# Optimization experiments

Measured on AMD Instinct MI355X. Metric: run time of the kernel, lower is better.

## Reference

```python
import jax, jax.numpy as jnp
import numpy as np
import math

B, N, DIM = 2, 4096, 1024
H, D, M = 16, 64, 256


def setup_inputs() -> dict:
    key = jax.random.key(0)
    ks = jax.random.split(key, 6)
    s = 1.0 / math.sqrt(DIM)
    return {
        "x": jax.random.normal(ks[0], (B, N, DIM), dtype=jnp.float32),
        "w_q": jax.random.normal(ks[1], (DIM, H * D), dtype=jnp.float32) * s,
        "w_k": jax.random.normal(ks[2], (DIM, H * D), dtype=jnp.float32) * s,
        "w_v": jax.random.normal(ks[3], (DIM, H * D), dtype=jnp.float32) * s,
        "w_o": jax.random.normal(ks[4], (H * D, DIM), dtype=jnp.float32) * s,
        "b_o": jnp.zeros((DIM,), dtype=jnp.float32),
        "omega": jax.random.normal(ks[5], (M, D), dtype=jnp.float32),
    }


def _heads(t):
    # [B, N, H*D] -> [B, H, N, D]
    return t.reshape(B, N, H, D).transpose(0, 2, 1, 3)


def _phi(t, omega):
    # t: [B,H,N,D], omega: [M,D] -> [B,H,N,M]
    proj = jnp.einsum("bhnd,md->bhnm", t, omega)
    norm = 0.5 * jnp.sum(t * t, axis=-1, keepdims=True)
    return jnp.exp(proj - norm) / math.sqrt(M)


def reference(x, w_q, w_k, w_v, w_o, b_o, omega):
    q = _heads(x @ w_q)
    k = _heads(x @ w_k)
    v = _heads(x @ w_v)
    phi_q = _phi(q, omega)          # [B,H,N,M]
    phi_k = _phi(k, omega)          # [B,H,N,M]
    kv = jnp.einsum("bhnm,bhnd->bhmd", phi_k, v)   # [B,H,M,D]
    k_sum = phi_k.sum(axis=2)                       # [B,H,M]
    z = 1.0 / (jnp.einsum("bhnm,bhm->bhn", phi_q, k_sum) + 1e-6)
    out = jnp.einsum("bhnm,bhmd->bhnd", phi_q, kv) * z[..., None]
    out = out.transpose(0, 2, 1, 3).reshape(B, N, H * D)
    return out @ w_o + b_o
```

## Files before the change

kernel.cpp:

```cpp
#include <hip/hip_runtime.h>

#define DEVI __device__ __forceinline__

using f32x4 = __attribute__((ext_vector_type(4))) float;
using fvec4 = __attribute__((ext_vector_type(4))) float;
using s16x4 = __attribute__((ext_vector_type(4))) short;
using s16x8 = __attribute__((ext_vector_type(8))) short;

DEVI unsigned short f2bf_rn(float f) {
  union { float f; unsigned u; } v; v.f = f;
  unsigned r = v.u + 0x7fffu + ((v.u >> 16) & 1u);
  return (unsigned short)(r >> 16);
}
DEVI float bf2f(unsigned short h) {
  union { unsigned u; float f; } v; v.u = ((unsigned)h) << 16;
  return v.f;
}
DEVI f32x4 mfma16(s16x8 a, s16x8 b, f32x4 c) {
  return __builtin_amdgcn_mfma_f32_16x16x32_bf16(a, b, c, 0, 0, 0);
}
DEVI void gld16(const void* g, void* lds) {
  __builtin_amdgcn_global_load_lds(
      (const __attribute__((address_space(1))) unsigned int*)g,
      (__attribute__((address_space(3))) unsigned int*)lds, 16, 0, 0);
}

__global__ __launch_bounds__(256) void k_split_x(
    const float* __restrict__ X,
    unsigned short* __restrict__ XH, unsigned short* __restrict__ XL)
{
  size_t i = ((size_t)blockIdx.x * 256 + threadIdx.x) * 8;
  fvec4 a = *(const fvec4*)&X[i];
  fvec4 b = *(const fvec4*)&X[i + 4];
  s16x8 hv, lv;
#pragma unroll
  for (int j = 0; j < 4; ++j) {
    unsigned short h = f2bf_rn(a[j]);
    hv[j] = (short)h; lv[j] = (short)f2bf_rn(a[j] - bf2f(h));
  }
#pragma unroll
  for (int j = 0; j < 4; ++j) {
    unsigned short h = f2bf_rn(b[j]);
    hv[4 + j] = (short)h; lv[4 + j] = (short)f2bf_rn(b[j] - bf2f(h));
  }
  *(s16x8*)&XH[i] = hv;
  *(s16x8*)&XL[i] = lv;
}

__global__ __launch_bounds__(256) void k_prep_w(
    const float* __restrict__ wq, const float* __restrict__ wk,
    const float* __restrict__ wv, const float* __restrict__ wo,
    const float* __restrict__ omega,
    unsigned short* __restrict__ WTh, unsigned short* __restrict__ WOT,
    unsigned short* __restrict__ OMB)
{
  __shared__ float tile[64][65];
  const int z = blockIdx.z;
  const int t = threadIdx.x;
  if (z == 4) {
    int bid = blockIdx.x * 16 + blockIdx.y;
    if (bid < 16) {
      int i = (bid * 256 + t) * 4;
      fvec4 v = *(const fvec4*)&omega[i];
      s16x4 hv;
#pragma unroll
      for (int q = 0; q < 4; ++q) hv[q] = (short)f2bf_rn(v[q]);
      *(s16x4*)&OMB[i] = hv;
    }
    return;
  }
  const float* src = (z == 0) ? wq : (z == 1) ? wk : (z == 2) ? wv : wo;
  const int k0 = blockIdx.x * 64;
  const int n0 = blockIdx.y * 64;
#pragma unroll
  for (int j = 0; j < 4; ++j) {
    int r = (t >> 4) + 16 * j;
    int c = (t & 15) * 4;
    fvec4 v = *(const fvec4*)&src[(size_t)(k0 + r) * 1024 + n0 + c];
#pragma unroll
    for (int i = 0; i < 4; ++i) tile[r][c + i] = v[i];
  }
  __syncthreads();
#pragma unroll
  for (int j = 0; j < 4; ++j) {
    int n = (t >> 4) + 16 * j;
    int kc = (t & 15) * 4;
    s16x4 hv;
#pragma unroll
    for (int i = 0; i < 4; ++i) hv[i] = (short)f2bf_rn(tile[kc + i][n]);
    if (z < 3) {
      *(s16x4*)&WTh[(size_t)(z * 1024 + n0 + n) * 1024 + k0 + kc] = hv;
    } else {
      *(s16x4*)&WOT[(size_t)(n0 + n) * 1024 + k0 + kc] = hv;
    }
  }
}

__global__ __launch_bounds__(256) void k_gemm_qkv(
    const unsigned short* __restrict__ XH, const unsigned short* __restrict__ XL,
    const unsigned short* __restrict__ WTh,
    unsigned short* __restrict__ QH, unsigned short* __restrict__ QL,
    unsigned short* __restrict__ KH, unsigned short* __restrict__ KL,
    unsigned short* __restrict__ VB)
{
  __shared__ unsigned short AH[3][128 * 32];
  __shared__ unsigned short BHs[3][128 * 32];
  __shared__ unsigned short AL[3][128 * 32];
  const int flat = blockIdx.y * 24 + blockIdx.x;
  const int swz = (flat & 7) * 192 + (flat >> 3);
  const int cb = swz % 24;
  const int rb = swz / 24;
  const int t = threadIdx.x;
  const int w = t >> 6, l = t & 63;
  const bool tp = (cb < 16);
  f32x4 acc[4][4];
#pragma unroll
  for (int a = 0; a < 4; ++a)
#pragma unroll
    for (int b = 0; b < 4; ++b) acc[a][b] = (f32x4)0.f;

  const int r0 = w * 32;
  const int lrow = l >> 2;
  const int lcol = (l & 3) * 8;
  const size_t gA = (size_t)(rb * 128 + r0 + lrow) * 1024 + lcol;
  const size_t gB = (size_t)(cb * 128 + r0 + lrow) * 1024 + lcol;
  const int lds0 = r0 * 32;
  const int lds1 = (r0 + 16) * 32;

  const int wm = (w & 1) * 64, wn = (w >> 1) * 64;
  const int lr = l & 15, ko = (l >> 4) * 8;

  auto STAGE = [&](int buf, int k0) {
    gld16(&XH[gA + k0], &AH[buf][lds0]);
    gld16(&XH[gA + (size_t)16 * 1024 + k0], &AH[buf][lds1]);
    if (tp) {
      gld16(&XL[gA + k0], &AL[buf][lds0]);
      gld16(&XL[gA + (size_t)16 * 1024 + k0], &AL[buf][lds1]);
    }
    gld16(&WTh[gB + k0], &BHs[buf][lds0]);
    gld16(&WTh[gB + (size_t)16 * 1024 + k0], &BHs[buf][lds1]);
  };

  STAGE(0, 0);
  STAGE(1, 32);
  int cur = 0;
  for (int ks = 0; ks < 32; ++ks) {
    if (ks < 30) {
      int nxt = (cur >= 1) ? cur - 1 : 2;
      STAGE(nxt, (ks + 2) * 32);
      if (tp) asm volatile("s_waitcnt vmcnt(12)" ::: "memory");
      else    asm volatile("s_waitcnt vmcnt(8)" ::: "memory");
    } else if (ks == 30) {
      if (tp) asm volatile("s_waitcnt vmcnt(6)" ::: "memory");
      else    asm volatile("s_waitcnt vmcnt(4)" ::: "memory");
    } else {
      asm volatile("s_waitcnt vmcnt(0)" ::: "memory");
    }
    __builtin_amdgcn_s_barrier();
    asm volatile("" ::: "memory");
    s16x8 ah[4], al[4], bh[4];
#pragma unroll
    for (int f = 0; f < 4; ++f) {
      ah[f] = *(const s16x8*)&AH[cur][(wm + f * 16 + lr) * 32 + ko];
      bh[f] = *(const s16x8*)&BHs[cur][(wn + f * 16 + lr) * 32 + ko];
    }
    if (tp) {
#pragma unroll
      for (int f = 0; f < 4; ++f) al[f] = *(const s16x8*)&AL[cur][(wm + f * 16 + lr) * 32 + ko];
    }
#pragma unroll
    for (int fa = 0; fa < 4; ++fa)
#pragma unroll
      for (int fb = 0; fb < 4; ++fb) {
        acc[fa][fb] = mfma16(ah[fa], bh[fb], acc[fa][fb]);
        if (tp) acc[fa][fb] = mfma16(al[fa], bh[fb], acc[fa][fb]);
      }
    asm volatile("s_waitcnt lgkmcnt(0)" ::: "memory");
    __builtin_amdgcn_s_barrier();
    asm volatile("" ::: "memory");
    cur = (cur < 2) ? cur + 1 : 0;
  }
  const int lg = l >> 4;
#pragma unroll
  for (int fa = 0; fa < 4; ++fa)
#pragma unroll
    for (int r = 0; r < 4; ++r) {
      int row = rb * 128 + wm + fa * 16 + lg * 4 + r;
#pragma unroll
      for (int fb = 0; fb < 4; ++fb) {
        int col = cb * 128 + wn + fb * 16 + lr;
        float v = acc[fa][fb][r];
        if (tp) {
          unsigned short hs = f2bf_rn(v);
          unsigned short ls = f2bf_rn(v - bf2f(hs));
          if (cb < 8) {
            QH[(size_t)row * 1024 + col] = hs;
            QL[(size_t)row * 1024 + col] = ls;
          } else {
            KH[(size_t)row * 1024 + col - 1024] = hs;
            KL[(size_t)row * 1024 + col - 1024] = ls;
          }
        } else {
          VB[(size_t)row * 1024 + col - 2048] = f2bf_rn(v);
        }
      }
    }
}

__global__ __launch_bounds__(512, 1) void k_phik_kv(
    const unsigned short* __restrict__ KH, const unsigned short* __restrict__ KL,
    const unsigned short* __restrict__ VB,
    const unsigned short* __restrict__ OMB, float* __restrict__ KVP)
{
  __shared__ unsigned short OH[256][72];
  __shared__ unsigned short KHs[64][72], KLs[64][72];
  __shared__ unsigned short PKT[256][72];
  __shared__ unsigned short AVT[80][72];
  __shared__ float norm_s[64];
  const int nc = blockIdx.x;
  const int bh = blockIdx.y;
  const int b = bh >> 4, h = bh & 15;
  const int t = threadIdx.x, w = t >> 6, l = t & 63;
  const int lr = l & 15, lg = l >> 4, ko8 = lg * 8;

#pragma unroll
  for (int j = 0; j < 4; ++j) {
    int idx = j * 512 + t;
    int m = idx >> 3, c = (idx & 7) * 8;
    *(s16x8*)&OH[m][c] = *(const s16x8*)&OMB[m * 64 + c];
  }
  for (int e = t; e < 16 * 64; e += 512) {
    int rr = e >> 6, cc = e & 63;
    AVT[64 + rr][cc] = (rr == 0) ? (unsigned short)0x3F80 : (unsigned short)0;
  }

  f32x4 acc2[5][2];
#pragma unroll
  for (int a = 0; a < 5; ++a)
#pragma unroll
    for (int bb = 0; bb < 2; ++bb) acc2[a][bb] = (f32x4)0.f;

  for (int st = 0; st < 8; ++st) {
    const int n0 = nc * 512 + st * 64;
    __syncthreads();
    {
      int r = t >> 3, c8 = (t & 7) * 8;
      size_t o = (size_t)(b * 4096 + n0 + r) * 1024 + h * 64 + c8;
      s16x8 vh = *(const s16x8*)&KH[o];
      s16x8 vl = *(const s16x8*)&KL[o];
      *(s16x8*)&KHs[r][c8] = vh;
      *(s16x8*)&KLs[r][c8] = vl;
      float ss = 0.f;
#pragma unroll
      for (int i = 0; i < 8; ++i) {
        float q = bf2f((unsigned short)vh[i]) + bf2f((unsigned short)vl[i]);
        ss += q * q;
      }
      ss += __shfl_xor(ss, 1);
      ss += __shfl_xor(ss, 2);
      ss += __shfl_xor(ss, 4);
      if ((t & 7) == 0) norm_s[r] = 0.5f * ss;
    }
    {
      int n = t >> 3, dq = (t & 7) * 8;
      s16x8 v = *(const s16x8*)&VB[(size_t)(b * 4096 + n0 + n) * 1024 + h * 64 + dq];
#pragma unroll
      for (int i = 0; i < 8; ++i) AVT[dq + i][n] = (unsigned short)v[i];
    }
    __syncthreads();
    f32x4 acc[4][2];
#pragma unroll
    for (int a = 0; a < 4; ++a)
#pragma unroll
      for (int bb = 0; bb < 2; ++bb) acc[a][bb] = (f32x4)0.f;
#pragma unroll
    for (int ksub = 0; ksub < 2; ++ksub) {
      int ko = ksub * 32 + ko8;
      s16x8 ah[4], al[4], bh[2];
#pragma unroll
      for (int f = 0; f < 4; ++f) {
        ah[f] = *(const s16x8*)&KHs[f * 16 + lr][ko];
        al[f] = *(const s16x8*)&KLs[f * 16 + lr][ko];
      }
#pragma unroll
      for (int f = 0; f < 2; ++f) bh[f] = *(const s16x8*)&OH[w * 32 + f * 16 + lr][ko];
#pragma unroll
      for (int fa = 0; fa < 4; ++fa)
#pragma unroll
        for (int fb = 0; fb < 2; ++fb) {
          acc[fa][fb] = mfma16(ah[fa], bh[fb], acc[fa][fb]);
          acc[fa][fb] = mfma16(al[fa], bh[fb], acc[fa][fb]);
        }
    }
#pragma unroll
    for (int fa = 0; fa < 4; ++fa)
#pragma unroll
      for (int r = 0; r < 4; ++r) {
        int n = fa * 16 + lg * 4 + r;
        float nm = norm_s[n];
#pragma unroll
        for (int fb = 0; fb < 2; ++fb) {
          int m = w * 32 + fb * 16 + lr;
          float p = __expf(acc[fa][fb][r] - nm) * 0.0625f;
          PKT[m][n] = f2bf_rn(p);
        }
      }
    __syncthreads();
#pragma unroll
    for (int ksub = 0; ksub < 2; ++ksub) {
      int ko = ksub * 32 + ko8;
      s16x8 fA[5], fB[2];
#pragma unroll
      for (int f = 0; f < 5; ++f) fA[f] = *(const s16x8*)&AVT[f * 16 + lr][ko];
#pragma unroll
      for (int f = 0; f < 2; ++f) fB[f] = *(const s16x8*)&PKT[w * 32 + f * 16 + lr][ko];
#pragma unroll
      for (int fa = 0; fa < 5; ++fa)
#pragma unroll
        for (int fb = 0; fb < 2; ++fb) acc2[fa][fb] = mfma16(fA[fa], fB[fb], acc2[fa][fb]);
    }
  }
#pragma unroll
  for (int fa = 0; fa < 5; ++fa)
#pragma unroll
    for (int r = 0; r < 4; ++r) {
      int dp = fa * 16 + lg * 4 + r;
#pragma unroll
      for (int fb = 0; fb < 2; ++fb) {
        int m = w * 32 + fb * 16 + lr;
        KVP[(size_t)((bh * 8 + nc) * 80 + dp) * 256 + m] = acc2[fa][fb][r];
      }
    }
}

__global__ __launch_bounds__(256) void k_kv_reduce(
    const float* __restrict__ KVP, unsigned short* __restrict__ KVTB)
{
  int idx = blockIdx.x * 256 + threadIdx.x;
  if (idx >= 32 * 80 * 256) return;
  int bh = idx / (80 * 256);
  int rem = idx % (80 * 256);
  float s = 0.f;
#pragma unroll
  for (int nci = 0; nci < 8; ++nci) s += KVP[(size_t)(bh * 8 + nci) * 80 * 256 + rem];
  KVTB[idx] = f2bf_rn(s);
}

__global__ __launch_bounds__(256) void k_phiq_attn(
    const unsigned short* QH, const unsigned short* QL,
    const unsigned short* __restrict__ OMB,
    const unsigned short* __restrict__ KVTB,
    unsigned short* ATT)
{
  __shared__ unsigned short QHs[64][72], QLs[64][72];
  __shared__ unsigned short OH[256][72];
  __shared__ unsigned short PQ[64][264];
  __shared__ unsigned short KVB[80][264];
  __shared__ float norm_s[64];
  const int nt = blockIdx.x;
  const int bh = blockIdx.y;
  const int t = threadIdx.x, w = t >> 6, l = t & 63;
  const int b = bh >> 4, h = bh & 15;
  const int lr = l & 15, lg = l >> 4, ko8 = lg * 8;

  {
    int r = t >> 2, cq = (t & 3) * 4;
    float ss = 0.f;
#pragma unroll
    for (int j = 0; j < 4; ++j) {
      int c = cq + 16 * j;
      size_t o = (size_t)(b * 4096 + nt * 64 + r) * 1024 + h * 64 + c;
      s16x4 vh = *(const s16x4*)&QH[o];
      s16x4 vl = *(const s16x4*)&QL[o];
      *(s16x4*)&QHs[r][c] = vh;
      *(s16x4*)&QLs[r][c] = vl;
#pragma unroll
      for (int i = 0; i < 4; ++i) {
        float q = bf2f((unsigned short)vh[i]) + bf2f((unsigned short)vl[i]);
        ss += q * q;
      }
    }
    ss += __shfl_xor(ss, 1);
    ss += __shfl_xor(ss, 2);
    if ((t & 3) == 0) norm_s[r] = 0.5f * ss;
  }
#pragma unroll
  for (int j = 0; j < 8; ++j) {
    int idx = j * 256 + t;
    int m = idx >> 3, c = (idx & 7) * 8;
    *(s16x8*)&OH[m][c] = *(const s16x8*)&OMB[m * 64 + c];
  }
#pragma unroll
  for (int j = 0; j < 10; ++j) {
    int e = (j * 256 + t) * 8;
    int dp = e >> 8, m = e & 255;
    *(s16x8*)&KVB[dp][m] = *(const s16x8*)&KVTB[(size_t)bh * 80 * 256 + dp * 256 + m];
  }
  __syncthreads();
  f32x4 acc[4][4];
#pragma unroll
  for (int a = 0; a < 4; ++a)
#pragma unroll
    for (int bb = 0; bb < 4; ++bb) acc[a][bb] = (f32x4)0.f;
#pragma unroll
  for (int ksub = 0; ksub < 2; ++ksub) {
    int ko = ksub * 32 + ko8;
    s16x8 ah[4], al[4], bh[4];
#pragma unroll
    for (int f = 0; f < 4; ++f) {
      ah[f] = *(const s16x8*)&QHs[f * 16 + lr][ko];
      al[f] = *(const s16x8*)&QLs[f * 16 + lr][ko];
      bh[f] = *(const s16x8*)&OH[w * 64 + f * 16 + lr][ko];
    }
#pragma unroll
    for (int fa = 0; fa < 4; ++fa)
#pragma unroll
      for (int fb = 0; fb < 4; ++fb) {
        acc[fa][fb] = mfma16(ah[fa], bh[fb], acc[fa][fb]);
        acc[fa][fb] = mfma16(al[fa], bh[fb], acc[fa][fb]);
      }
  }
#pragma unroll
  for (int fa = 0; fa < 4; ++fa)
#pragma unroll
    for (int r = 0; r < 4; ++r) {
      int n = fa * 16 + lg * 4 + r;
      float nm = norm_s[n];
#pragma unroll
      for (int fb = 0; fb < 4; ++fb) {
        int m = w * 64 + fb * 16 + lr;
        float p = __expf(acc[fa][fb][r] - nm) * 0.0625f;
        PQ[n][m] = f2bf_rn(p);
      }
    }
  __syncthreads();
  f32x4 acc2[5];
#pragma unroll
  for (int bb = 0; bb < 5; ++bb) acc2[bb] = (f32x4)0.f;
  for (int ks = 0; ks < 8; ++ks) {
    const int m0 = ks * 32;
    s16x8 fA = *(const s16x8*)&PQ[w * 16 + lr][m0 + ko8];
    s16x8 fB[5];
#pragma unroll
    for (int f = 0; f < 5; ++f) fB[f] = *(const s16x8*)&KVB[f * 16 + lr][m0 + ko8];
#pragma unroll
    for (int fb = 0; fb < 5; ++fb) acc2[fb] = mfma16(fA, fB[fb], acc2[fb]);
  }
#pragma unroll
  for (int r = 0; r < 4; ++r) {
    float den = __shfl(acc2[4][r], (l & 48));
    float z = 1.f / (den + 1e-6f);
    int n = nt * 64 + w * 16 + lg * 4 + r;
#pragma unroll
    for (int fb = 0; fb < 4; ++fb) {
      int col = h * 64 + fb * 16 + lr;
      ATT[(size_t)(b * 4096 + n) * 1024 + col] = f2bf_rn(acc2[fb][r] * z);
    }
  }
}

__global__ __launch_bounds__(256) void k_gemm_out(
    const unsigned short* __restrict__ ATT,
    const unsigned short* __restrict__ WOT,
    const float* __restrict__ b_o,
    float* __restrict__ OUT)
{
  __shared__ unsigned short As[3][128 * 32], Bs[3][128 * 32];
  const int flat = blockIdx.y * 8 + blockIdx.x;
  const int swz = (flat & 7) * 64 + (flat >> 3);
  const int cb = swz % 8;
  const int rb = swz / 8;
  const int t = threadIdx.x, w = t >> 6, l = t & 63;
  f32x4 acc[4][4];
#pragma unroll
  for (int a = 0; a < 4; ++a)
#pragma unroll
    for (int bb = 0; bb < 4; ++bb) acc[a][bb] = (f32x4)0.f;

  const int r0 = w * 32;
  const int lrow = l >> 2;
  const int lcol = (l & 3) * 8;
  const size_t gA = (size_t)(rb * 128 + r0 + lrow) * 1024 + lcol;
  const size_t gB = (size_t)(cb * 128 + r0 + lrow) * 1024 + lcol;
  const int lds0 = r0 * 32;
  const int lds1 = (r0 + 16) * 32;

  const int wm = (w & 1) * 64, wn = (w >> 1) * 64;
  const int lr = l & 15, ko = (l >> 4) * 8;

  auto STAGE = [&](int buf, int k0) {
    gld16(&ATT[gA + k0], &As[buf][lds0]);
    gld16(&ATT[gA + (size_t)16 * 1024 + k0], &As[buf][lds1]);
    gld16(&WOT[gB + k0], &Bs[buf][lds0]);
    gld16(&WOT[gB + (size_t)16 * 1024 + k0], &Bs[buf][lds1]);
  };

  STAGE(0, 0);
  STAGE(1, 32);
  int cur = 0;
  for (int ks = 0; ks < 32; ++ks) {
    if (ks < 30) {
      int nxt = (cur >= 1) ? cur - 1 : 2;
      STAGE(nxt, (ks + 2) * 32);
      asm volatile("s_waitcnt vmcnt(8)" ::: "memory");
    } else if (ks == 30) {
      asm volatile("s_waitcnt vmcnt(4)" ::: "memory");
    } else {
      asm volatile("s_waitcnt vmcnt(0)" ::: "memory");
    }
    __builtin_amdgcn_s_barrier();
    asm volatile("" ::: "memory");
    s16x8 fA[4], fB[4];
#pragma unroll
    for (int f = 0; f < 4; ++f) {
      fA[f] = *(const s16x8*)&As[cur][(wm + f * 16 + lr) * 32 + ko];
      fB[f] = *(const s16x8*)&Bs[cur][(wn + f * 16 + lr) * 32 + ko];
    }
#pragma unroll
    for (int fa = 0; fa < 4; ++fa)
#pragma unroll
      for (int fb = 0; fb < 4; ++fb) acc[fa][fb] = mfma16(fA[fa], fB[fb], acc[fa][fb]);
    asm volatile("s_waitcnt lgkmcnt(0)" ::: "memory");
    __builtin_amdgcn_s_barrier();
    asm volatile("" ::: "memory");
    cur = (cur < 2) ? cur + 1 : 0;
  }
  const int lg = l >> 4;
#pragma unroll
  for (int fa = 0; fa < 4; ++fa)
#pragma unroll
    for (int r = 0; r < 4; ++r) {
      int row = rb * 128 + wm + fa * 16 + lg * 4 + r;
#pragma unroll
      for (int fb = 0; fb < 4; ++fb) {
        int col = cb * 128 + wn + fb * 16 + lr;
        OUT[(size_t)row * 1024 + col] = acc[fa][fb][r] + b_o[col];
      }
    }
}

extern "C" void kernel_launch(void* const* d_in, const int* in_sizes, int n_in,
                              void* d_out, int out_size, void* d_ws, size_t ws_size,
                              hipStream_t stream)
{
  const float* x  = (const float*)d_in[0];
  const float* wq = (const float*)d_in[1];
  const float* wk = (const float*)d_in[2];
  const float* wv = (const float*)d_in[3];
  const float* wo = (const float*)d_in[4];
  const float* bo = (const float*)d_in[5];
  const float* om = (const float*)d_in[6];
  float* out = (float*)d_out;

  const size_t PLANE = (size_t)8192 * 1024 * 2;
  char* ws = (char*)d_ws;
  unsigned short* WOT = (unsigned short*)(ws);
  char* segB = ws + 2097152;
  char* segC = segB + 2 * PLANE;
  char* segD = segC + 4 * PLANE;
  char* segE = segD + 26214400;

  unsigned short* QH  = (unsigned short*)segB;
  unsigned short* QL  = (unsigned short*)(segB + PLANE);
  unsigned short* ATT = (unsigned short*)segB;

  unsigned short* KH  = (unsigned short*)segC;
  unsigned short* KL  = (unsigned short*)(segC + PLANE);
  unsigned short* VB  = (unsigned short*)(segC + 2 * PLANE);
  unsigned short* XH  = (unsigned short*)(segC + 3 * PLANE);

  unsigned short* WTh = (unsigned short*)segD;
  unsigned short* XL  = (unsigned short*)(segD + 6291456);
  float* KVP = (float*)segD;
  unsigned short* KVTB = (unsigned short*)segE;
  unsigned short* OMB  = (unsigned short*)(segE + 1310720);

  k_split_x<<<dim3(4096), 256, 0, stream>>>(x, XH, XL);
  k_prep_w<<<dim3(16, 16, 5), 256, 0, stream>>>(wq, wk, wv, wo, om, WTh, WOT, OMB);
  k_gemm_qkv<<<dim3(24, 64), 256, 0, stream>>>(XH, XL, WTh, QH, QL, KH, KL, VB);
  k_phik_kv<<<dim3(8, 32), 512, 0, stream>>>(KH, KL, VB, OMB, KVP);
  k_kv_reduce<<<dim3(2560), 256, 0, stream>>>(KVP, KVTB);
  k_phiq_attn<<<dim3(64, 32), 256, 0, stream>>>(QH, QL, OMB, KVTB, ATT);
  k_gemm_out<<<dim3(8, 64), 256, 0, stream>>>(ATT, WOT, bo, out);
}
```

Baseline: 242.3 us.

## Shrink QKV GEMM to double buffering and load omega/KV fragments directly to registers

The QKV GEMM drops from a three-stage to a two-stage LDS ring, which lowers LDS use but shortens how far global loads run ahead of compute. In the phi_k and phi_q kernels, omega MFMA fragments now load straight from global memory into registers, so the OH shared tiles are gone. In the phi_q attention kernel, KV fragments are read from global/L2 inside the k-loop instead of being staged in LDS. This cuts LDS footprint and staging cost, which may raise occupancy, at the price of more global loads with less latency hiding.

```diff
diff --git a/kernel.cpp b/kernel.cpp
--- a/kernel.cpp
+++ b/kernel.cpp
@@ -103,9 +103,9 @@
     unsigned short* __restrict__ KH, unsigned short* __restrict__ KL,
     unsigned short* __restrict__ VB)
 {
-  __shared__ unsigned short AH[3][128 * 32];
-  __shared__ unsigned short BHs[3][128 * 32];
-  __shared__ unsigned short AL[3][128 * 32];
+  __shared__ unsigned short AH[2][128 * 32];
+  __shared__ unsigned short BHs[2][128 * 32];
+  __shared__ unsigned short AL[2][128 * 32];
   const int flat = blockIdx.y * 24 + blockIdx.x;
   const int swz = (flat & 7) * 192 + (flat >> 3);
   const int cb = swz % 24;
@@ -142,15 +142,10 @@
   };
 
   STAGE(0, 0);
-  STAGE(1, 32);
   int cur = 0;
   for (int ks = 0; ks < 32; ++ks) {
-    if (ks < 30) {
-      int nxt = (cur >= 1) ? cur - 1 : 2;
-      STAGE(nxt, (ks + 2) * 32);
-      if (tp) asm volatile("s_waitcnt vmcnt(12)" ::: "memory");
-      else    asm volatile("s_waitcnt vmcnt(8)" ::: "memory");
-    } else if (ks == 30) {
+    if (ks < 31) {
+      STAGE(cur ^ 1, (ks + 1) * 32);
       if (tp) asm volatile("s_waitcnt vmcnt(6)" ::: "memory");
       else    asm volatile("s_waitcnt vmcnt(4)" ::: "memory");
     } else {
@@ -178,7 +173,7 @@
     asm volatile("s_waitcnt lgkmcnt(0)" ::: "memory");
     __builtin_amdgcn_s_barrier();
     asm volatile("" ::: "memory");
-    cur = (cur < 2) ? cur + 1 : 0;
+    cur ^= 1;
   }
   const int lg = l >> 4;
 #pragma unroll
@@ -212,7 +207,6 @@
     const unsigned short* __restrict__ VB,
     const unsigned short* __restrict__ OMB, float* __restrict__ KVP)
 {
-  __shared__ unsigned short OH[256][72];
   __shared__ unsigned short KHs[64][72], KLs[64][72];
   __shared__ unsigned short PKT[256][72];
   __shared__ unsigned short AVT[80][72];
@@ -223,12 +217,13 @@
   const int t = threadIdx.x, w = t >> 6, l = t & 63;
   const int lr = l & 15, lg = l >> 4, ko8 = lg * 8;
 
-#pragma unroll
-  for (int j = 0; j < 4; ++j) {
-    int idx = j * 512 + t;
-    int m = idx >> 3, c = (idx & 7) * 8;
-    *(s16x8*)&OH[m][c] = *(const s16x8*)&OMB[m * 64 + c];
-  }
+  s16x8 omf[2][2];
+#pragma unroll
+  for (int ksub = 0; ksub < 2; ++ksub)
+#pragma unroll
+    for (int f = 0; f < 2; ++f)
+      omf[ksub][f] = *(const s16x8*)&OMB[(w * 32 + f * 16 + lr) * 64 + ksub * 32 + ko8];
+
   for (int e = t; e < 16 * 64; e += 512) {
     int rr = e >> 6, cc = e & 63;
     AVT[64 + rr][cc] = (rr == 0) ? (unsigned short)0x3F80 : (unsigned short)0;
@@ -276,20 +271,18 @@
 #pragma unroll
     for (int ksub = 0; ksub < 2; ++ksub) {
       int ko = ksub * 32 + ko8;
-      s16x8 ah[4], al[4], bh[2];
+      s16x8 ah[4], al[4];
 #pragma unroll
       for (int f = 0; f < 4; ++f) {
         ah[f] = *(const s16x8*)&KHs[f * 16 + lr][ko];
         al[f] = *(const s16x8*)&KLs[f * 16 + lr][ko];
       }
 #pragma unroll
-      for (int f = 0; f < 2; ++f) bh[f] = *(const s16x8*)&OH[w * 32 + f * 16 + lr][ko];
-#pragma unroll
       for (int fa = 0; fa < 4; ++fa)
 #pragma unroll
         for (int fb = 0; fb < 2; ++fb) {
-          acc[fa][fb] = mfma16(ah[fa], bh[fb], acc[fa][fb]);
-          acc[fa][fb] = mfma16(al[fa], bh[fb], acc[fa][fb]);
+          acc[fa][fb] = mfma16(ah[fa], omf[ksub][fb], acc[fa][fb]);
+          acc[fa][fb] = mfma16(al[fa], omf[ksub][fb], acc[fa][fb]);
         }
     }
 #pragma unroll
@@ -353,15 +346,20 @@
     unsigned short* ATT)
 {
   __shared__ unsigned short QHs[64][72], QLs[64][72];
-  __shared__ unsigned short OH[256][72];
   __shared__ unsigned short PQ[64][264];
-  __shared__ unsigned short KVB[80][264];
   __shared__ float norm_s[64];
   const int nt = blockIdx.x;
   const int bh = blockIdx.y;
   const int t = threadIdx.x, w = t >> 6, l = t & 63;
   const int b = bh >> 4, h = bh & 15;
   const int lr = l & 15, lg = l >> 4, ko8 = lg * 8;
+
+  s16x8 omf[2][4];
+#pragma unroll
+  for (int ksub = 0; ksub < 2; ++ksub)
+#pragma unroll
+    for (int f = 0; f < 4; ++f)
+      omf[ksub][f] = *(const s16x8*)&OMB[(w * 64 + f * 16 + lr) * 64 + ksub * 32 + ko8];
 
   {
     int r = t >> 2, cq = (t & 3) * 4;
@@ -384,18 +382,6 @@
     ss += __shfl_xor(ss, 2);
     if ((t & 3) == 0) norm_s[r] = 0.5f * ss;
   }
-#pragma unroll
-  for (int j = 0; j < 8; ++j) {
-    int idx = j * 256 + t;
-    int m = idx >> 3, c = (idx & 7) * 8;
-    *(s16x8*)&OH[m][c] = *(const s16x8*)&OMB[m * 64 + c];
-  }
-#pragma unroll
-  for (int j = 0; j < 10; ++j) {
-    int e = (j * 256 + t) * 8;
-    int dp = e >> 8, m = e & 255;
-    *(s16x8*)&KVB[dp][m] = *(const s16x8*)&KVTB[(size_t)bh * 80 * 256 + dp * 256 + m];
-  }
   __syncthreads();
   f32x4 acc[4][4];
 #pragma unroll
@@ -405,19 +391,18 @@
 #pragma unroll
   for (int ksub = 0; ksub < 2; ++ksub) {
     int ko = ksub * 32 + ko8;
-    s16x8 ah[4], al[4], bh[4];
+    s16x8 ah[4], al[4];
 #pragma unroll
     for (int f = 0; f < 4; ++f) {
       ah[f] = *(const s16x8*)&QHs[f * 16 + lr][ko];
       al[f] = *(const s16x8*)&QLs[f * 16 + lr][ko];
-      bh[f] = *(const s16x8*)&OH[w * 64 + f * 16 + lr][ko];
     }
 #pragma unroll
     for (int fa = 0; fa < 4; ++fa)
 #pragma unroll
       for (int fb = 0; fb < 4; ++fb) {
-        acc[fa][fb] = mfma16(ah[fa], bh[fb], acc[fa][fb]);
-        acc[fa][fb] = mfma16(al[fa], bh[fb], acc[fa][fb]);
+        acc[fa][fb] = mfma16(ah[fa], omf[ksub][fb], acc[fa][fb]);
+        acc[fa][fb] = mfma16(al[fa], omf[ksub][fb], acc[fa][fb]);
       }
   }
 #pragma unroll
@@ -434,6 +419,7 @@
       }
     }
   __syncthreads();
+  const size_t kvbase = (size_t)bh * 80 * 256;
   f32x4 acc2[5];
 #pragma unroll
   for (int bb = 0; bb < 5; ++bb) acc2[bb] = (f32x4)0.f;
@@ -442,7 +428,8 @@
     s16x8 fA = *(const s16x8*)&PQ[w * 16 + lr][m0 + ko8];
     s16x8 fB[5];
 #pragma unroll
-    for (int f = 0; f < 5; ++f) fB[f] = *(const s16x8*)&KVB[f * 16 + lr][m0 + ko8];
+    for (int f = 0; f < 5; ++f)
+      fB[f] = *(const s16x8*)&KVTB[kvbase + (size_t)(f * 16 + lr) * 256 + m0 + ko8];
 #pragma unroll
     for (int fb = 0; fb < 5; ++fb) acc2[fb] = mfma16(fA, fB[fb], acc2[fb]);
   }
```

Result: faster. 228.2 us (-5.8%).
